# Performance work log

Hardware: AMD Instinct MI355X
Metric: run time of the kernel (lower is better)

The kernel has to match this reference:

```python
import jax, jax.numpy as jnp
import numpy as np

B, L, H, NL, NRES = 64, 2048, 64, 10, 3
EPS = 1e-5


def _conv1d(x, w, b, pad):
    # x: [B, C, L], w: [O, I, K] (torch layout)
    y = jax.lax.conv_general_dilated(x, w, window_strides=(1,), padding=[(pad, pad)],
                                     dimension_numbers=("NCH", "OIH", "NCH"))
    return y + b[None, :, None]


def _bn(x, g, b, m, v):
    # eval-mode BatchNorm1d over channel dim of [B, C, L]
    scale = (g * jax.lax.rsqrt(v + EPS))[None, :, None]
    return (x - m[None, :, None]) * scale + b[None, :, None]


def _lstm_layer(x, w_ih, w_hh, b_ih, b_hh):
    # x: [T, B, H]; gate order (torch): i, f, g, o
    gates_x = jnp.einsum("tbh,gh->tbg", x, w_ih) + (b_ih + b_hh)  # [T, B, 4H]

    def step(carry, gx):
        h, c = carry
        gates = gx + h @ w_hh.T
        i, f, g, o = jnp.split(gates, 4, axis=-1)
        c = jax.nn.sigmoid(f) * c + jax.nn.sigmoid(i) * jnp.tanh(g)
        h = jax.nn.sigmoid(o) * jnp.tanh(c)
        return (h, c), h

    nb = x.shape[1]
    init = (jnp.zeros((nb, H), x.dtype), jnp.zeros((nb, H), x.dtype))
    _, hs = jax.lax.scan(step, init, gates_x)
    return hs  # [T, B, H]


def setup_inputs() -> dict:
    key = jax.random.key(0)
    ks = jax.random.split(key, 24)
    r = lambda i, shape, s=0.05: jax.random.normal(ks[i], shape, jnp.float32) * s
    inp = {
        "input": jax.random.normal(ks[0], (B, L, 4), jnp.float32),
        "mc": jax.random.uniform(ks[1], (B,), dtype=jnp.float32),
        "conv1_w": r(2, (32, 4, 1), 0.3), "conv1_b": r(3, (32,)),
        "conv2_w": r(4, (64, 32, 1), 0.2), "conv2_b": r(5, (64,)),
        "res_bn1_g": jnp.ones((NRES, 64), jnp.float32), "res_bn1_b": jnp.zeros((NRES, 64), jnp.float32),
        "res_bn1_m": jnp.zeros((NRES, 64), jnp.float32), "res_bn1_v": jnp.ones((NRES, 64), jnp.float32),
        "res_conv1_w": r(6, (NRES, 64, 64, 11)), "res_conv1_b": r(7, (NRES, 64)),
        "res_bn2_g": jnp.ones((NRES, 64), jnp.float32), "res_bn2_b": jnp.zeros((NRES, 64), jnp.float32),
        "res_bn2_m": jnp.zeros((NRES, 64), jnp.float32), "res_bn2_v": jnp.ones((NRES, 64), jnp.float32),
        "res_conv2_w": r(8, (NRES, 64, 64, 11)), "res_conv2_b": r(9, (NRES, 64)),
        "lstm_w_ih": r(10, (NL, 4 * H, H), 0.1), "lstm_w_hh": r(11, (NL, 4 * H, H), 0.1),
        "lstm_b_ih": r(12, (NL, 4 * H)), "lstm_b_hh": r(13, (NL, 4 * H)),
        "out_w": r(14, (H, 2), 0.1), "out_b": r(15, (2,)),
        "l": L,
    }
    return inp


def reference(input, mc, conv1_w, conv1_b, conv2_w, conv2_b,
              res_bn1_g, res_bn1_b, res_bn1_m, res_bn1_v, res_conv1_w, res_conv1_b,
              res_bn2_g, res_bn2_b, res_bn2_m, res_bn2_v, res_conv2_w, res_conv2_b,
              lstm_w_ih, lstm_w_hh, lstm_b_ih, lstm_b_hh, out_w, out_b, l):
    # mc and l are computed/accepted but never used by the original forward.
    x = jnp.transpose(input, (0, 2, 1))                    # [B, 4, L]
    x = jax.nn.relu(_conv1d(x, conv1_w, conv1_b, 0))       # [B, 32, L]
    x = jax.nn.relu(_conv1d(x, conv2_w, conv2_b, 0))       # [B, 64, L]
    for i in range(NRES):                                  # 3 pre-activation residual units
        h = jax.nn.relu(_bn(x, res_bn1_g[i], res_bn1_b[i], res_bn1_m[i], res_bn1_v[i]))
        h = _conv1d(h, res_conv1_w[i], res_conv1_b[i], 5)
        h = jax.nn.relu(_bn(h, res_bn2_g[i], res_bn2_b[i], res_bn2_m[i], res_bn2_v[i]))
        h = _conv1d(h, res_conv2_w[i], res_conv2_b[i], 5)
        x = x + h
    x = jnp.transpose(x, (2, 0, 1))                        # [L, B, 64] (seq-first, like torch LSTM)
    for layer in range(NL):
        x = _lstm_layer(x, lstm_w_ih[layer], lstm_w_hh[layer], lstm_b_ih[layer], lstm_b_hh[layer])
    logits = x[-1] @ out_w + out_b                         # [B, 2]
    return jax.nn.log_softmax(logits, axis=1)
```

## Files before the change

kernel.cpp:

```cpp
#include <hip/hip_runtime.h>
#include <hip/hip_bf16.h>

#define TL 2048
#define NB 64
#define NH 64
#define NLAY 10
#define NRESU 3
#define RSTEP 64

typedef float f32x4 __attribute__((ext_vector_type(4)));
typedef unsigned u32x2 __attribute__((ext_vector_type(2)));
typedef short bhalf8 __attribute__((ext_vector_type(8)));

__device__ __forceinline__ unsigned short f2bf(float f) {
    unsigned u = __float_as_uint(f);
    unsigned r = u + 0x7fffu + ((u >> 16) & 1u);
    return (unsigned short)(r >> 16);
}
__device__ __forceinline__ float bf2f(unsigned short h) {
    return __uint_as_float(((unsigned)h) << 16);
}
__device__ __forceinline__ float fast_sigmoid(float x) {
    return __builtin_amdgcn_rcpf(1.0f + __expf(-x));
}
__device__ __forceinline__ float fast_tanh(float x) {
    float e = __expf(2.0f * x);
    return 1.0f - 2.0f * __builtin_amdgcn_rcpf(e + 1.0f);
}

__global__ __launch_bounds__(256) void k_frontend(
    const float* __restrict__ in,
    const float* __restrict__ c1w, const float* __restrict__ c1b,
    const float* __restrict__ c2w, const float* __restrict__ c2b,
    float* __restrict__ x0)
{
    __shared__ float s_c1w[128];
    __shared__ float s_c1b[32];
    __shared__ float s_c2w[64 * 33];
    __shared__ float s_c2b[64];
    __shared__ float h1[64 * 33];
    __shared__ float ot[64 * 65];
    int tid = threadIdx.x;
    int b = blockIdx.x >> 5;
    int l0 = (blockIdx.x & 31) << 6;
    if (tid < 128) s_c1w[tid] = c1w[tid];
    if (tid < 32) s_c1b[tid] = c1b[tid];
    if (tid < 64) s_c2b[tid] = c2b[tid];
    for (int r = tid; r < 2048; r += 256) s_c2w[(r >> 5) * 33 + (r & 31)] = c2w[r];
    __syncthreads();
    if (tid < 64) {
        const float* ip = in + ((size_t)b * TL + l0 + tid) * 4;
        float x0v = ip[0], x1 = ip[1], x2 = ip[2], x3 = ip[3];
#pragma unroll
        for (int o = 0; o < 32; o++) {
            float a = s_c1w[o * 4 + 0] * x0v + s_c1w[o * 4 + 1] * x1 +
                      s_c1w[o * 4 + 2] * x2 + s_c1w[o * 4 + 3] * x3 + s_c1b[o];
            h1[tid * 33 + o] = fmaxf(a, 0.0f);
        }
    }
    __syncthreads();
    {
        int o = tid & 63, lg = tid >> 6;
#pragma unroll
        for (int j = 0; j < 16; j++) {
            int l = lg * 16 + j;
            float a = s_c2b[o];
#pragma unroll
            for (int i = 0; i < 32; i++) a += h1[l * 33 + i] * s_c2w[o * 33 + i];
            ot[o * 65 + l] = fmaxf(a, 0.0f);
        }
    }
    __syncthreads();
    for (int r = 0; r < 16; r++) {
        int idx = tid + 256 * r;
        int c = idx >> 6, l = idx & 63;
        x0[((size_t)b * 64 + c) * TL + l0 + l] = ot[c * 65 + l];
    }
}

__global__ __launch_bounds__(256) void k_prepw_mfma(
    const float* __restrict__ w, unsigned short* __restrict__ wbh, unsigned short* __restrict__ wbl)
{
    int idx = blockIdx.x * 256 + threadIdx.x;
    if (idx >= NRESU * 11 * 64 * 64) return;
    int i = idx & 63;
    int rest = idx >> 6;
    int o = rest & 63;
    rest >>= 6;
    int k = rest % 11;
    int u = rest / 11;
    float v = w[(((size_t)u * 64 + o) * 64 + i) * 11 + k];
    unsigned short hb = f2bf(v);
    float lo = v - bf2f(hb);
    wbh[idx] = hb;
    wbl[idx] = f2bf(lo);
}

__global__ __launch_bounds__(256) void k_resconv_mfma(
    const float* __restrict__ in, float* __restrict__ out,
    const unsigned short* __restrict__ wbh, const unsigned short* __restrict__ wbl,
    const float* __restrict__ bias,
    const float* __restrict__ bg, const float* __restrict__ bb,
    const float* __restrict__ bm, const float* __restrict__ bv,
    int accumulate)
{
    __shared__ float sscale[64], sshift[64];
    __shared__ __align__(16) char smem[41472];
    unsigned short* XTH = (unsigned short*)smem;
    unsigned short* XTL = XTH + 144 * 72;
    float* Yb = (float*)smem;

    int tid = threadIdx.x;
    int b = blockIdx.x >> 4;
    int l0 = (blockIdx.x & 15) << 7;
    int lane = tid & 63;
    int wv = tid >> 6;
    int l15 = lane & 15, l4 = lane >> 4;

    if (tid < 64) {
        float sc = bg[tid] * rsqrtf(bv[tid] + 1e-5f);
        sscale[tid] = sc;
        sshift[tid] = bb[tid] - bm[tid] * sc;
    }
    __syncthreads();

    {
        int i = tid >> 2, ll0 = (tid & 3) * 36;
        float sc = sscale[i], sh = sshift[i];
        const float* ip = in + ((size_t)b * 64 + i) * TL;
#pragma unroll
        for (int j = 0; j < 36; j++) {
            int ll = ll0 + j;
            int l = l0 - 5 + ll;
            float v = 0.0f;
            if (l >= 0 && l < TL) v = fmaxf(ip[l] * sc + sh, 0.0f);
            unsigned short hb = f2bf(v);
            float lo = v - bf2f(hb);
            XTH[ll * 72 + i] = hb;
            XTL[ll * 72 + i] = f2bf(lo);
        }
    }
    __syncthreads();

    f32x4 acc[2][4];
#pragma unroll
    for (int s = 0; s < 2; s++)
#pragma unroll
        for (int ot = 0; ot < 4; ot++) acc[s][ot] = (f32x4){0, 0, 0, 0};

    for (int k = 0; k < 11; k++) {
#pragma unroll
        for (int ic = 0; ic < 2; ic++) {
            bhalf8 ah[2], al[2];
#pragma unroll
            for (int s = 0; s < 2; s++) {
                int row = (wv * 2 + s) * 16 + l15 + k;
                ah[s] = *(const bhalf8*)&XTH[row * 72 + ic * 32 + l4 * 8];
                al[s] = *(const bhalf8*)&XTL[row * 72 + ic * 32 + l4 * 8];
            }
#pragma unroll
            for (int ot = 0; ot < 4; ot++) {
                size_t woff = ((size_t)(k * 64 + ot * 16 + l15)) * 64 + ic * 32 + l4 * 8;
                bhalf8 bh = *(const bhalf8*)&wbh[woff];
                bhalf8 bl = *(const bhalf8*)&wbl[woff];
#pragma unroll
                for (int s = 0; s < 2; s++) {
                    acc[s][ot] = __builtin_amdgcn_mfma_f32_16x16x32_bf16(ah[s], bh, acc[s][ot], 0, 0, 0);
                    acc[s][ot] = __builtin_amdgcn_mfma_f32_16x16x32_bf16(al[s], bh, acc[s][ot], 0, 0, 0);
                    acc[s][ot] = __builtin_amdgcn_mfma_f32_16x16x32_bf16(ah[s], bl, acc[s][ot], 0, 0, 0);
                }
            }
        }
    }
    __syncthreads();

#pragma unroll
    for (int s = 0; s < 2; s++)
#pragma unroll
        for (int ot = 0; ot < 4; ot++)
#pragma unroll
            for (int r = 0; r < 4; r++)
                Yb[((wv * 2 + s) * 16 + l4 * 4 + r) * 66 + ot * 16 + l15] = acc[s][ot][r];
    __syncthreads();

    {
        int o = tid >> 2, ls0 = (tid & 3) * 32;
        float bsv = bias[o];
        float* op = out + ((size_t)b * 64 + o) * TL + l0 + ls0;
        if (accumulate) {
#pragma unroll
            for (int j = 0; j < 32; j++) op[j] += Yb[(ls0 + j) * 66 + o] + bsv;
        } else {
#pragma unroll
            for (int j = 0; j < 32; j++) op[j] = Yb[(ls0 + j) * 66 + o] + bsv;
        }
    }
}

__global__ __launch_bounds__(256) void k_transpose(
    const float* __restrict__ x0, unsigned short* __restrict__ Xbf)
{
    __shared__ float t[64 * 65];
    int tid = threadIdx.x;
    int b = blockIdx.x >> 5;
    int t0 = (blockIdx.x & 31) << 6;
    for (int r = 0; r < 16; r++) {
        int idx = tid + 256 * r;
        int c = idx >> 6, tt = idx & 63;
        t[c * 65 + tt] = x0[((size_t)b * 64 + c) * TL + t0 + tt];
    }
    __syncthreads();
    for (int r = 0; r < 16; r++) {
        int idx = tid + 256 * r;
        int tt = idx >> 6, c = idx & 63;
        Xbf[((size_t)(t0 + tt)) * (NB * NH) + b * 64 + c] = f2bf(t[c * 65 + tt]);
    }
}

__global__ __launch_bounds__(512) void k_lstm(
    const unsigned short* __restrict__ Xbf,
    const float* __restrict__ w_ih, const float* __restrict__ w_hh,
    const float* __restrict__ b_ih, const float* __restrict__ b_hh,
    unsigned short* __restrict__ ring, float* __restrict__ final_h, int* prog)
{
    int bid = blockIdx.x;
    int grp = bid & 7;
    int layer = bid >> 3;
    if (grp >= 4 || layer >= NLAY) return;
    int b0 = grp * 16;
    int tid = threadIdx.x;
    int w = tid >> 6;
    int lane = tid & 63;
    int l15 = lane & 15, l4 = lane >> 4;
    int self = layer * 4 + grp;
    const bool has_store = (layer < NLAY - 1);
    const bool use_ring = (layer > 0);
    int brow = tid >> 5;
    int cc0 = (tid & 31) * 2;
    int T0 = w * 2, T1 = w * 2 + 1;

    __shared__ __align__(16) unsigned short XH[2][16][136];
    __shared__ float gbuf[16][16][17];

    bhalf8 Bh[2][4];
#pragma unroll
    for (int s = 0; s < 2; s++) {
        int n = (w * 2 + s) * 16 + l15;
        const float* rih = w_ih + ((size_t)layer * 256 + n) * 64;
        const float* rhh = w_hh + ((size_t)layer * 256 + n) * 64;
#pragma unroll
        for (int kt = 0; kt < 4; kt++) {
#pragma unroll
            for (int j = 0; j < 8; j++) {
                int k = kt * 32 + l4 * 8 + j;
                float v = (k < 64) ? rih[k] : rhh[k - 64];
                Bh[s][kt][j] = (short)f2bf(v);
            }
        }
    }
    float bv[8];
#pragma unroll
    for (int g = 0; g < 4; g++) {
#pragma unroll
        for (int s = 0; s < 2; s++) {
            int n = g * 64 + cc0 + s;
            bv[g * 2 + s] = b_ih[layer * 256 + n] + b_hh[layer * 256 + n];
        }
    }
    for (int idx = tid; idx < 2 * 16 * 64; idx += 512) {
        XH[idx >> 10][(idx >> 6) & 15][64 + (idx & 63)] = 0;
    }
    float cst[2] = {0.f, 0.f};

    int* p_self = prog + self * 32;
    int* p_prev = prog + (self - 4) * 32;
    int* p_next = prog + (self + 4) * 32;
    int cached_prev = 0, cached_next = 0;

#define POLL_GE(ptr, tgt, cachev)                                                     \
    if (cachev < (tgt)) {                                                             \
        int v_; long g_ = 0;                                                          \
        while ((v_ = __hip_atomic_load(ptr, __ATOMIC_ACQUIRE,                         \
                        __HIP_MEMORY_SCOPE_AGENT)) < (tgt) && ++g_ < 1500000)         \
            __builtin_amdgcn_s_sleep(2);                                              \
        cachev = v_;                                                                  \
    }

    if (tid == 0 && layer > 0) { POLL_GE(p_prev, 32, cached_prev); }
    __syncthreads();
    unsigned px[4];
    {
        unsigned p0;
        if (!use_ring) {
            const unsigned short* s0 = Xbf + (size_t)(b0 + brow) * 64 + cc0;
            asm volatile("global_load_dword %0, %1, off" : "=&v"(p0) : "v"(s0) : "memory");
        } else {
            const unsigned short* s0 = ring + ((size_t)(layer - 1) * RSTEP) * 4096 + (b0 + brow) * 64 + cc0;
            asm volatile("global_load_dword %0, %1, off sc0 sc1" : "=&v"(p0) : "v"(s0) : "memory");
        }
        asm volatile("s_waitcnt vmcnt(0)" ::: "memory");
        __builtin_amdgcn_sched_barrier(0);
        *(unsigned*)&XH[0][brow][cc0] = p0;
#pragma unroll
        for (int pre = 1; pre <= 3; pre++) {
            if (!use_ring) {
                const unsigned short* sp = Xbf + ((size_t)pre * NB + b0 + brow) * 64 + cc0;
                asm volatile("global_load_dword %0, %1, off" : "=&v"(px[pre]) : "v"(sp) : "memory");
            } else {
                const unsigned short* sp = ring + ((size_t)(layer - 1) * RSTEP + pre) * 4096 + (b0 + brow) * 64 + cc0;
                asm volatile("global_load_dword %0, %1, off sc0 sc1" : "=&v"(px[pre]) : "v"(sp) : "memory");
            }
        }
    }
    asm volatile("s_waitcnt vmcnt(0)" ::: "memory");
    __builtin_amdgcn_sched_barrier(0);
    __syncthreads();

    for (int t0 = 0; t0 < TL; t0 += 8) {
#pragma unroll
        for (int ts = 0; ts < 8; ++ts) {
            const int p = ts & 1, q = p ^ 1;
            const int t = t0 + ts;
            const int cons = (ts + 1) & 3;
            const int pref = ts & 3;

            f32x4 Acc0 = {0, 0, 0, 0}, Acc1 = {0, 0, 0, 0};
#pragma unroll
            for (int kt = 0; kt < 4; kt++) {
                bhalf8 Ah = *(const bhalf8*)&XH[p][l15][kt * 32 + l4 * 8];
                Acc0 = __builtin_amdgcn_mfma_f32_16x16x32_bf16(Ah, Bh[0][kt], Acc0, 0, 0, 0);
                Acc1 = __builtin_amdgcn_mfma_f32_16x16x32_bf16(Ah, Bh[1][kt], Acc1, 0, 0, 0);
            }
#pragma unroll
            for (int r = 0; r < 4; r++) {
                gbuf[T0][l4 * 4 + r][l15] = Acc0[r];
                gbuf[T1][l4 * 4 + r][l15] = Acc1[r];
            }
            asm volatile("s_waitcnt lgkmcnt(0)" ::: "memory");
            __builtin_amdgcn_s_barrier();
            __builtin_amdgcn_sched_barrier(0);

            if (has_store) { asm volatile("s_waitcnt vmcnt(4)" ::: "memory"); }
            else           { asm volatile("s_waitcnt vmcnt(2)" ::: "memory"); }
            __builtin_amdgcn_sched_barrier(0);

            *(unsigned*)&XH[q][brow][cc0] = px[cons];

            int tb = cc0 >> 4, cb = cc0 & 15;
            float hv[2];
#pragma unroll
            for (int s = 0; s < 2; s++) {
                float gi = gbuf[0 * 4 + tb][brow][cb + s] + bv[0 + s];
                float gf = gbuf[1 * 4 + tb][brow][cb + s] + bv[2 + s];
                float gg = gbuf[2 * 4 + tb][brow][cb + s] + bv[4 + s];
                float go = gbuf[3 * 4 + tb][brow][cb + s] + bv[6 + s];
                float c = fast_sigmoid(gf) * cst[s] + fast_sigmoid(gi) * fast_tanh(gg);
                cst[s] = c;
                hv[s] = fast_sigmoid(go) * fast_tanh(c);
            }
            unsigned hw = ((unsigned)f2bf(hv[1]) << 16) | (unsigned)f2bf(hv[0]);

            *(unsigned*)&XH[q][brow][64 + cc0] = hw;
            if (has_store) {
                unsigned short* ap = ring + ((size_t)layer * RSTEP + (t & 63)) * 4096 + (b0 + brow) * 64 + cc0;
                asm volatile("global_store_dword %0, %1, off sc0 sc1" :: "v"(ap), "v"(hw) : "memory");
            } else if (t == TL - 1) {
                final_h[(b0 + brow) * NH + cc0] = hv[0];
                final_h[(b0 + brow) * NH + cc0 + 1] = hv[1];
            }

            {
                int tt = t + 4; if (tt > TL - 1) tt = TL - 1;
                if (!use_ring) {
                    const unsigned short* sp = Xbf + ((size_t)tt * NB + b0 + brow) * 64 + cc0;
                    asm volatile("global_load_dword %0, %1, off" : "=&v"(px[pref]) : "v"(sp) : "memory");
                } else {
                    const unsigned short* sp = ring + ((size_t)(layer - 1) * RSTEP + (tt & 63)) * 4096 + (b0 + brow) * 64 + cc0;
                    asm volatile("global_load_dword %0, %1, off sc0 sc1" : "=&v"(px[pref]) : "v"(sp) : "memory");
                }
            }

            asm volatile("s_waitcnt lgkmcnt(0)" ::: "memory");
            __builtin_amdgcn_s_barrier();
            __builtin_amdgcn_sched_barrier(0);
        }

        if (has_store) { asm volatile("s_waitcnt vmcnt(1)" ::: "memory"); }
        __builtin_amdgcn_s_barrier();
        __builtin_amdgcn_sched_barrier(0);
        if (tid == 0) {
            __hip_atomic_store(p_self, t0, __ATOMIC_RELEASE, __HIP_MEMORY_SCOPE_AGENT);
            int nt0 = t0 + 8;
            if (nt0 < TL) {
                if (use_ring) {
                    int tgt = nt0 + 16; if (tgt > TL) tgt = TL;
                    POLL_GE(p_prev, tgt, cached_prev);
                }
                if (has_store) {
                    int need = nt0 - 64;
                    if (need > 0) { POLL_GE(p_next, need, cached_next); }
                }
            }
        }
        __builtin_amdgcn_s_barrier();
        __builtin_amdgcn_sched_barrier(0);
    }

    asm volatile("s_waitcnt vmcnt(0)" ::: "memory");
    __builtin_amdgcn_s_barrier();
    if (tid == 0) {
        __hip_atomic_store(p_self, TL, __ATOMIC_RELEASE, __HIP_MEMORY_SCOPE_AGENT);
    }
#undef POLL_GE
}

__global__ void k_head(const float* __restrict__ fh, const float* __restrict__ ow,
                       const float* __restrict__ ob, float* __restrict__ out)
{
    int b = threadIdx.x;
    if (b >= NB) return;
    const float* h = fh + b * NH;
    float l0 = ob[0], l1 = ob[1];
    for (int uu = 0; uu < 64; uu++) { l0 += h[uu] * ow[uu * 2]; l1 += h[uu] * ow[uu * 2 + 1]; }
    float m = fmaxf(l0, l1);
    float s = expf(l0 - m) + expf(l1 - m);
    float ls = m + logf(s);
    out[b * 2] = l0 - ls;
    out[b * 2 + 1] = l1 - ls;
}

extern "C" void kernel_launch(void* const* d_in, const int* in_sizes, int n_in,
                              void* d_out, int out_size, void* d_ws, size_t ws_size,
                              hipStream_t stream) {
    const float* input = (const float*)d_in[0];
    const float* c1w = (const float*)d_in[2];
    const float* c1b = (const float*)d_in[3];
    const float* c2w = (const float*)d_in[4];
    const float* c2b = (const float*)d_in[5];
    const float* bn1g = (const float*)d_in[6];
    const float* bn1b = (const float*)d_in[7];
    const float* bn1m = (const float*)d_in[8];
    const float* bn1v = (const float*)d_in[9];
    const float* rw1 = (const float*)d_in[10];
    const float* rb1 = (const float*)d_in[11];
    const float* bn2g = (const float*)d_in[12];
    const float* bn2b = (const float*)d_in[13];
    const float* bn2m = (const float*)d_in[14];
    const float* bn2v = (const float*)d_in[15];
    const float* rw2 = (const float*)d_in[16];
    const float* rb2 = (const float*)d_in[17];
    const float* wih = (const float*)d_in[18];
    const float* whh = (const float*)d_in[19];
    const float* bih = (const float*)d_in[20];
    const float* bhh = (const float*)d_in[21];
    const float* outw = (const float*)d_in[22];
    const float* outb = (const float*)d_in[23];

    float* ws = (float*)d_ws;
    float*          x0buf = ws;
    float*          t1buf = x0buf + 8388608;
    unsigned short* Xbf   = (unsigned short*)(t1buf + 8388608);
    unsigned short* ringb = Xbf + 8388608;
    float*          fhbuf = (float*)(ringb + 2359296);
    int*            progb = (int*)(fhbuf + 4096);
    unsigned short* wbh1  = (unsigned short*)(progb + 40 * 32);
    unsigned short* wbl1  = wbh1 + NRESU * 11 * 64 * 64;
    unsigned short* wbh2  = wbl1 + NRESU * 11 * 64 * 64;
    unsigned short* wbl2  = wbh2 + NRESU * 11 * 64 * 64;

    hipMemsetAsync(progb, 0, 40 * 32 * sizeof(int), stream);

    k_prepw_mfma<<<528, 256, 0, stream>>>(rw1, wbh1, wbl1);
    k_prepw_mfma<<<528, 256, 0, stream>>>(rw2, wbh2, wbl2);
    k_frontend<<<2048, 256, 0, stream>>>(input, c1w, c1b, c2w, c2b, x0buf);
    for (int uu = 0; uu < NRESU; uu++) {
        k_resconv_mfma<<<1024, 256, 0, stream>>>(x0buf, t1buf, wbh1 + uu * 45056, wbl1 + uu * 45056,
                                                 rb1 + uu * 64, bn1g + uu * 64, bn1b + uu * 64,
                                                 bn1m + uu * 64, bn1v + uu * 64, 0);
        k_resconv_mfma<<<1024, 256, 0, stream>>>(t1buf, x0buf, wbh2 + uu * 45056, wbl2 + uu * 45056,
                                                 rb2 + uu * 64, bn2g + uu * 64, bn2b + uu * 64,
                                                 bn2m + uu * 64, bn2v + uu * 64, 1);
    }
    k_transpose<<<2048, 256, 0, stream>>>(x0buf, Xbf);
    k_lstm<<<80, 512, 0, stream>>>(Xbf, wih, whh, bih, bhh, ringb, fhbuf, progb);
    k_head<<<1, 64, 0, stream>>>(fhbuf, outw, outb, (float*)d_out);
}
```

Baseline: 2.832 ms.

## Compute LSTM gates in registers per wave, removing gate LDS exchange and barrier

Each wave now owns 16 hidden units and computes all four gates for them with four MFMAs per k-tile. The gate nonlinearities therefore run directly on the accumulators, with the bias folded into the accumulator init. This removes the gbuf shared-memory round trip and one barrier per timestep. Waves split the MFMA rows in halves, so pairs of waves (w and w+4) do duplicate MFMA work. Outputs are written as 16-bit shorts to LDS and global memory, which doubles the store count and changes the vmcnt wait threshold.

```diff
diff --git a/kernel.cpp b/kernel.cpp
--- a/kernel.cpp
+++ b/kernel.cpp
@@ -232,39 +232,33 @@
     int w = tid >> 6;
     int lane = tid & 63;
     int l15 = lane & 15, l4 = lane >> 4;
+    int w4 = w & 3;
+    int rhalf = w >> 2;
+    int u = w4 * 16 + l15;
     int self = layer * 4 + grp;
     const bool has_store = (layer < NLAY - 1);
     const bool use_ring = (layer > 0);
     int brow = tid >> 5;
     int cc0 = (tid & 31) * 2;
-    int T0 = w * 2, T1 = w * 2 + 1;
 
     __shared__ __align__(16) unsigned short XH[2][16][136];
-    __shared__ float gbuf[16][16][17];
-
-    bhalf8 Bh[2][4];
-#pragma unroll
-    for (int s = 0; s < 2; s++) {
-        int n = (w * 2 + s) * 16 + l15;
+
+    bhalf8 Bh[4][4];
+    float bv[4];
+#pragma unroll
+    for (int g = 0; g < 4; g++) {
+        int n = g * 64 + u;
         const float* rih = w_ih + ((size_t)layer * 256 + n) * 64;
         const float* rhh = w_hh + ((size_t)layer * 256 + n) * 64;
+        bv[g] = b_ih[layer * 256 + n] + b_hh[layer * 256 + n];
 #pragma unroll
         for (int kt = 0; kt < 4; kt++) {
 #pragma unroll
             for (int j = 0; j < 8; j++) {
                 int k = kt * 32 + l4 * 8 + j;
                 float v = (k < 64) ? rih[k] : rhh[k - 64];
-                Bh[s][kt][j] = (short)f2bf(v);
-            }
-        }
-    }
-    float bv[8];
-#pragma unroll
-    for (int g = 0; g < 4; g++) {
-#pragma unroll
-        for (int s = 0; s < 2; s++) {
-            int n = g * 64 + cc0 + s;
-            bv[g * 2 + s] = b_ih[layer * 256 + n] + b_hh[layer * 256 + n];
+                Bh[g][kt][j] = (short)f2bf(v);
+            }
         }
     }
     for (int idx = tid; idx < 2 * 16 * 64; idx += 512) {
@@ -324,49 +318,48 @@
             const int cons = (ts + 1) & 3;
             const int pref = ts & 3;
 
-            f32x4 Acc0 = {0, 0, 0, 0}, Acc1 = {0, 0, 0, 0};
+            f32x4 acc[4];
+#pragma unroll
+            for (int g = 0; g < 4; g++) acc[g] = (f32x4){bv[g], bv[g], bv[g], bv[g]};
 #pragma unroll
             for (int kt = 0; kt < 4; kt++) {
                 bhalf8 Ah = *(const bhalf8*)&XH[p][l15][kt * 32 + l4 * 8];
-                Acc0 = __builtin_amdgcn_mfma_f32_16x16x32_bf16(Ah, Bh[0][kt], Acc0, 0, 0, 0);
-                Acc1 = __builtin_amdgcn_mfma_f32_16x16x32_bf16(Ah, Bh[1][kt], Acc1, 0, 0, 0);
-            }
-#pragma unroll
-            for (int r = 0; r < 4; r++) {
-                gbuf[T0][l4 * 4 + r][l15] = Acc0[r];
-                gbuf[T1][l4 * 4 + r][l15] = Acc1[r];
-            }
-            asm volatile("s_waitcnt lgkmcnt(0)" ::: "memory");
-            __builtin_amdgcn_s_barrier();
-            __builtin_amdgcn_sched_barrier(0);
-
-            if (has_store) { asm volatile("s_waitcnt vmcnt(4)" ::: "memory"); }
+                acc[0] = __builtin_amdgcn_mfma_f32_16x16x32_bf16(Ah, Bh[0][kt], acc[0], 0, 0, 0);
+                acc[1] = __builtin_amdgcn_mfma_f32_16x16x32_bf16(Ah, Bh[1][kt], acc[1], 0, 0, 0);
+                acc[2] = __builtin_amdgcn_mfma_f32_16x16x32_bf16(Ah, Bh[2][kt], acc[2], 0, 0, 0);
+                acc[3] = __builtin_amdgcn_mfma_f32_16x16x32_bf16(Ah, Bh[3][kt], acc[3], 0, 0, 0);
+            }
+
+            float hv[2];
+            unsigned short hb[2];
+#pragma unroll
+            for (int rr = 0; rr < 2; rr++) {
+                int r = rhalf * 2 + rr;
+                float c = fast_sigmoid(acc[1][r]) * cst[rr] +
+                          fast_sigmoid(acc[0][r]) * fast_tanh(acc[2][r]);
+                cst[rr] = c;
+                float h = fast_sigmoid(acc[3][r]) * fast_tanh(c);
+                hv[rr] = h;
+                hb[rr] = f2bf(h);
+            }
+
+            if (has_store) { asm volatile("s_waitcnt vmcnt(6)" ::: "memory"); }
             else           { asm volatile("s_waitcnt vmcnt(2)" ::: "memory"); }
             __builtin_amdgcn_sched_barrier(0);
 
             *(unsigned*)&XH[q][brow][cc0] = px[cons];
 
-            int tb = cc0 >> 4, cb = cc0 & 15;
-            float hv[2];
-#pragma unroll
-            for (int s = 0; s < 2; s++) {
-                float gi = gbuf[0 * 4 + tb][brow][cb + s] + bv[0 + s];
-                float gf = gbuf[1 * 4 + tb][brow][cb + s] + bv[2 + s];
-                float gg = gbuf[2 * 4 + tb][brow][cb + s] + bv[4 + s];
-                float go = gbuf[3 * 4 + tb][brow][cb + s] + bv[6 + s];
-                float c = fast_sigmoid(gf) * cst[s] + fast_sigmoid(gi) * fast_tanh(gg);
-                cst[s] = c;
-                hv[s] = fast_sigmoid(go) * fast_tanh(c);
-            }
-            unsigned hw = ((unsigned)f2bf(hv[1]) << 16) | (unsigned)f2bf(hv[0]);
-
-            *(unsigned*)&XH[q][brow][64 + cc0] = hw;
-            if (has_store) {
-                unsigned short* ap = ring + ((size_t)layer * RSTEP + (t & 63)) * 4096 + (b0 + brow) * 64 + cc0;
-                asm volatile("global_store_dword %0, %1, off sc0 sc1" :: "v"(ap), "v"(hw) : "memory");
-            } else if (t == TL - 1) {
-                final_h[(b0 + brow) * NH + cc0] = hv[0];
-                final_h[(b0 + brow) * NH + cc0 + 1] = hv[1];
+#pragma unroll
+            for (int rr = 0; rr < 2; rr++) {
+                int b = l4 * 4 + rhalf * 2 + rr;
+                XH[q][b][64 + u] = hb[rr];
+                if (has_store) {
+                    unsigned short* ap = ring + ((size_t)layer * RSTEP + (t & 63)) * 4096 + (b0 + b) * 64 + u;
+                    unsigned val = hb[rr];
+                    asm volatile("global_store_short %0, %1, off sc0 sc1" :: "v"(ap), "v"(val) : "memory");
+                } else if (t == TL - 1) {
+                    final_h[(b0 + b) * NH + u] = hv[rr];
+                }
             }
 
             {
```

Result: no change. 2.805 ms (-0.9%).
